# Performance work log

Measured on AMD Instinct MI355X. Metric: run time of the kernel, lower is better.

The kernel has to match this reference:

```python
import jax, jax.numpy as jnp
import numpy as np

N = 50000      # nodes
E = 800000     # edges (avg degree 16)
F = 6          # input node features
C = 64         # conv_hidden_channels
M = 256        # mlp_hidden_channels
NCLS = 24      # num_classes
EPS = 1e-5     # BatchNorm eps


def _bn(h, g, b):
    # BatchNorm1d in training mode: biased batch stats over the batch axis
    mu = h.mean(axis=0)
    var = ((h - mu) ** 2).mean(axis=0)
    return g * (h - mu) * jax.lax.rsqrt(var + EPS) + b


def _block(x, W, b, g, beta):
    # Lin -> ReLU -> BN  (one MLP block)
    return _bn(jax.nn.relu(x @ W + b), g, beta)


def _edge_conv(x, src, dst, Wa, ba, ga, bea, Wb, bb, gb, beb):
    # EdgeConv: message = MLP([x_i, x_j - x_i]), max-aggregated onto target i
    xi = x[dst]                                   # [E, d]
    xj = x[src]                                   # [E, d]
    e = jnp.concatenate([xi, xj - xi], axis=-1)   # [E, 2d]
    h = _block(_block(e, Wa, ba, ga, bea), Wb, bb, gb, beb)  # [E, C]
    agg = jax.ops.segment_max(h, dst, num_segments=N)        # [N, C]
    return jnp.where(jnp.isfinite(agg), agg, 0.0)  # zero-fill isolated nodes


def setup_inputs() -> dict:
    key = jax.random.key(0)
    ks = jax.random.split(key, 12)

    def w(k, shape, fan_in):
        return jax.random.normal(k, shape, jnp.float32) * (1.0 / np.sqrt(fan_in))

    z = lambda *s: jnp.zeros(s, jnp.float32)
    o = lambda *s: jnp.ones(s, jnp.float32)

    x = jax.random.normal(ks[0], (N, F), jnp.float32)
    edge_index = jax.random.randint(ks[1], (2, E), 0, N, jnp.int32)

    return {
        "x": x,
        # conv1 MLP: Lin(2F,C)+BN, Lin(C,C)+BN
        "W1a": w(ks[2], (2 * F, C), 2 * F), "b1a": z(C), "g1a": o(C), "be1a": z(C),
        "W1b": w(ks[3], (C, C), C),         "b1b": z(C), "g1b": o(C), "be1b": z(C),
        # conv2/conv3 stacked: Lin(2C,C)+BN, Lin(C,C)+BN
        "Wa": w(ks[4], (2, 2 * C, C), 2 * C), "ba": z(2, C), "ga": o(2, C), "bea": z(2, C),
        "Wb": w(ks[5], (2, C, C), C),         "bb": z(2, C), "gb": o(2, C), "beb": z(2, C),
        # lin1: Lin(3C, M)+BN
        "Wl": w(ks[6], (3 * C, M), 3 * C), "bl": z(M), "gl": o(M), "bel": z(M),
        # head: Lin(M, M/4)+BN, Lin(M/4, M/8)+BN, Lin(M/8, NCLS)
        "Wm1": w(ks[7], (M, M // 4), M),      "bm1": z(M // 4), "gm1": o(M // 4), "bem1": z(M // 4),
        "Wm2": w(ks[8], (M // 4, M // 8), M // 4), "bm2": z(M // 8), "gm2": o(M // 8), "bem2": z(M // 8),
        "Wo": w(ks[9], (M // 8, NCLS), M // 8), "bo": z(NCLS),
        "edge_index": edge_index,
    }


def reference(x, W1a, b1a, g1a, be1a, W1b, b1b, g1b, be1b,
              Wa, ba, ga, bea, Wb, bb, gb, beb,
              Wl, bl, gl, bel,
              Wm1, bm1, gm1, bem1, Wm2, bm2, gm2, bem2,
              Wo, bo, edge_index):
    src, dst = edge_index[0], edge_index[1]
    x1 = _edge_conv(x,  src, dst, W1a, b1a, g1a, be1a, W1b, b1b, g1b, be1b)
    x2 = _edge_conv(x1, src, dst, Wa[0], ba[0], ga[0], bea[0], Wb[0], bb[0], gb[0], beb[0])
    x3 = _edge_conv(x2, src, dst, Wa[1], ba[1], ga[1], bea[1], Wb[1], bb[1], gb[1], beb[1])
    h = _block(jnp.concatenate([x1, x2, x3], axis=-1), Wl, bl, gl, bel)
    h = _block(h, Wm1, bm1, gm1, bem1)   # Dropout is identity (eval)
    h = _block(h, Wm2, bm2, gm2, bem2)   # Dropout is identity (eval)
    logits = h @ Wo + bo
    return jax.nn.log_softmax(logits, axis=1)
```

## Files before the change

kernel.cpp:

```cpp
#include <hip/hip_runtime.h>
#include <hip/hip_bf16.h>

#define EPS 1e-5f
typedef unsigned short bfr;
typedef unsigned short hfr;
typedef _Float16 h2v __attribute__((ext_vector_type(2)));
typedef _Float16 f16x8 __attribute__((ext_vector_type(8)));
typedef float f32x4 __attribute__((ext_vector_type(4)));

#if defined(__has_builtin)
#if __has_builtin(__builtin_amdgcn_fdot2)
#define HAS_FDOT2 1
#endif
#endif

static inline int cdiv(int a, int b){ return (a + b - 1) / b; }

__device__ __forceinline__ float bf2f(bfr u){ return __uint_as_float((unsigned)u << 16); }
__device__ __forceinline__ bfr f2bf(float f){
  unsigned u = __float_as_uint(f);
  u += 0x7fffu + ((u >> 16) & 1u);
  return (bfr)(u >> 16);
}
__device__ __forceinline__ unsigned pack2bf(float a, float b){
  return (unsigned)f2bf(a) | ((unsigned)f2bf(b) << 16);
}
__device__ __forceinline__ float h2f(hfr u){ _Float16 h; __builtin_memcpy(&h, &u, 2); return (float)h; }
__device__ __forceinline__ _Float16 asH(hfr u){ _Float16 h; __builtin_memcpy(&h, &u, 2); return h; }
__device__ __forceinline__ hfr f2h(float f){ _Float16 h = (_Float16)f; hfr u; __builtin_memcpy(&u, &h, 2); return u; }
__device__ __forceinline__ unsigned pack2h(float a, float b){
  return (unsigned)f2h(a) | ((unsigned)f2h(b) << 16);
}
__device__ __forceinline__ h2v u2h2(unsigned u){ h2v r; __builtin_memcpy(&r, &u, 4); return r; }
__device__ __forceinline__ unsigned h22u(h2v h){ unsigned u; __builtin_memcpy(&u, &h, 4); return u; }
__device__ __forceinline__ float dot2(h2v a, h2v b, float c){
#ifdef HAS_FDOT2
  return __builtin_amdgcn_fdot2(a, b, c, false);
#else
  return c + (float)a.x * (float)b.x + (float)a.y * (float)b.y;
#endif
}

__global__ __launch_bounds__(256) void detect_kernel(const bfr* __restrict__ xr, int nwords, int* __restrict__ flag){
  int i = threadIdx.x;
  int bad = 0;
  if (i < nwords){
    bfr lo = xr[2 * i];
    int e = (lo >> 7) & 0xFF;
    bool plausible = ((lo & 0x7FFF) == 0) || (e >= 97 && e <= 157);
    bad = plausible ? 0 : 1;
  }
  __shared__ int s[256];
  s[threadIdx.x] = bad; __syncthreads();
  for (int st = 128; st; st >>= 1){
    if (threadIdx.x < st) s[threadIdx.x] += s[threadIdx.x + st];
    __syncthreads();
  }
  if (threadIdx.x == 0) *flag = (s[0] > 32) ? 1 : 0;
}

#define NPAR 31
struct ParamPtrs { const void* p[NPAR]; };
struct ParamOfs  { int off[NPAR + 1]; };

__global__ __launch_bounds__(256) void acvt_batch_kernel(ParamPtrs pp, ParamOfs po,
                                                         float* __restrict__ out, int total,
                                                         const int* __restrict__ flag){
  int g = blockIdx.x * 256 + threadIdx.x;
  if (g >= total) return;
  int isf = *flag;
  int t = 0;
  while (po.off[t + 1] <= g) ++t;
  int i = g - po.off[t];
  out[g] = isf ? ((const float*)pp.p[t])[i] : bf2f(((const bfr*)pp.p[t])[i]);
}

__global__ __launch_bounds__(256) void deg_kernel(const int* __restrict__ dst, int* __restrict__ deg, int E){
  int e = blockIdx.x * 256 + threadIdx.x;
  if (e < E) atomicAdd(&deg[dst[e]], 1);
}

__global__ __launch_bounds__(256) void scan1_kernel(const int* __restrict__ deg, int* __restrict__ locoff,
                                                    int* __restrict__ bsum, int N){
  __shared__ int s[256];
  int i = blockIdx.x * 256 + threadIdx.x;
  int v = (i < N) ? deg[i] : 0;
  s[threadIdx.x] = v; __syncthreads();
  for (int st = 1; st < 256; st <<= 1){
    int u = (threadIdx.x >= st) ? s[threadIdx.x - st] : 0;
    __syncthreads();
    s[threadIdx.x] += u;
    __syncthreads();
  }
  if (i < N) locoff[i] = s[threadIdx.x] - v;
  if (threadIdx.x == 255) bsum[blockIdx.x] = s[255];
}

__global__ __launch_bounds__(256) void scan2_kernel(int* __restrict__ bsum, int nb){
  __shared__ int s[256];
  const int t = threadIdx.x;
  int carry = 0;
  for (int base = 0; base < nb; base += 256){
    int v = (base + t < nb) ? bsum[base + t] : 0;
    s[t] = v; __syncthreads();
    for (int st = 1; st < 256; st <<= 1){
      int u = (t >= st) ? s[t - st] : 0;
      __syncthreads();
      s[t] += u;
      __syncthreads();
    }
    if (base + t < nb) bsum[base + t] = carry + s[t] - v;
    carry += s[255];
    __syncthreads();
  }
}

__global__ __launch_bounds__(256) void scan3_kernel(const int* __restrict__ locoff, const int* __restrict__ bsum,
                                                    int* __restrict__ row_off, int* __restrict__ cur,
                                                    int N, int E){
  int i = blockIdx.x * 256 + threadIdx.x;
  if (i < N){
    int v = locoff[i] + bsum[blockIdx.x];
    row_off[i] = v; cur[i] = v;
  }
  if (i == 0) row_off[N] = E;
}

__global__ __launch_bounds__(256) void scatter_kernel(const int* __restrict__ src, const int* __restrict__ dst,
                                                      int* __restrict__ cur, int* __restrict__ ssrc,
                                                      int* __restrict__ sdst, int E){
  int e = blockIdx.x * 256 + threadIdx.x;
  if (e < E){
    int d = dst[e];
    int p = atomicAdd(&cur[d], 1);
    ssrc[p] = src[e];
    sdst[p] = d;
  }
}

template<bool FIRST>
__global__ __launch_bounds__(256) void gemmPQ_kernel(const void* __restrict__ Av, int lda,
                                                     const float* __restrict__ Wa, int d,
                                                     const float* __restrict__ ba,
                                                     hfr* __restrict__ P, hfr* __restrict__ Q, int N){
  __shared__ unsigned WsU[64 * 64];
  const int y = blockIdx.y;
  const int tot = d * 64;
  if (FIRST){
    float* Ws = (float*)WsU;
    for (int i = threadIdx.x; i < tot; i += 256)
      Ws[i] = y ? Wa[tot + i] : (Wa[i] - Wa[tot + i]);
  } else {
    for (int i = threadIdx.x; i < 32 * 64; i += 256){
      int p = i >> 6, c = i & 63;
      int i0 = (2 * p) * 64 + c, i1 = (2 * p + 1) * 64 + c;
      float w0 = y ? Wa[tot + i0] : (Wa[i0] - Wa[tot + i0]);
      float w1 = y ? Wa[tot + i1] : (Wa[i1] - Wa[tot + i1]);
      WsU[i] = pack2h(w0, w1);
    }
  }
  __syncthreads();
  const int row = blockIdx.x * 256 + threadIdx.x;
  if (row >= N) return;
  float acc[64];
#pragma unroll
  for (int c = 0; c < 64; ++c) acc[c] = 0.f;
  if (FIRST){
    const float* Ws = (const float*)WsU;
    const float* Af = (const float*)Av + (size_t)row * lda;
    for (int k = 0; k < d; ++k){
      float a = Af[k];
      const float* wr = Ws + k * 64;
#pragma unroll
      for (int c4 = 0; c4 < 16; ++c4){
        float4 w = *(const float4*)(wr + 4 * c4);
        acc[4*c4+0] += a * w.x; acc[4*c4+1] += a * w.y;
        acc[4*c4+2] += a * w.z; acc[4*c4+3] += a * w.w;
      }
    }
  } else {
    const hfr* Ah = (const hfr*)Av + (size_t)row * lda;
#pragma unroll
    for (int k8 = 0; k8 < 8; ++k8){
      uint4 av = *(const uint4*)(Ah + k8 * 8);
      unsigned pr[4] = {av.x, av.y, av.z, av.w};
#pragma unroll
      for (int pi = 0; pi < 4; ++pi){
        h2v ap = u2h2(pr[pi]);
        const unsigned* wr = WsU + (k8 * 4 + pi) * 64;
#pragma unroll
        for (int c = 0; c < 64; ++c) acc[c] = dot2(ap, u2h2(wr[c]), acc[c]);
      }
    }
  }
  if (!y){
#pragma unroll
    for (int c = 0; c < 64; ++c) acc[c] += ba[c];
  }
  unsigned p[32];
#pragma unroll
  for (int c = 0; c < 64; c += 2) p[c / 2] = pack2h(acc[c], acc[c + 1]);
  hfr* outp = (y ? Q : P) + (size_t)row * 64;
  uint4* op = (uint4*)outp;
#pragma unroll
  for (int i = 0; i < 8; ++i) op[i] = make_uint4(p[4*i], p[4*i+1], p[4*i+2], p[4*i+3]);
}

template<int NOUT, bool FOLD>
__global__ __launch_bounds__(256) void gemm_kernel(const hfr* __restrict__ Ah, int lda,
                                                   const float* __restrict__ W, int ldw,
                                                   const float* __restrict__ bias,
                                                   const float* __restrict__ stats, float cntInv,
                                                   const float* __restrict__ g, const float* __restrict__ be,
                                                   hfr* __restrict__ Ov, int ldo,
                                                   int nrows, int K, int relu){
  __shared__ unsigned Wp[32 * NOUT];
  __shared__ float aS[256], bbS[256], bfull[NOUT], bsum[256];
  const int ct = blockIdx.y * NOUT;
  const int tid = threadIdx.x;
  if (FOLD){
    for (int k = tid; k < K; k += 256){
      float mu = stats[k] * cntInv;
      float var = stats[K + k] * cntInv - mu * mu;
      float ai = g[k] * rsqrtf(var + EPS);
      aS[k] = ai; bbS[k] = be[k] - ai * mu;
    }
    __syncthreads();
    constexpr int parts = 256 / NOUT;
    int c = tid % NOUT, p = tid / NOUT;
    float s = 0.f;
    for (int k = p; k < K; k += parts) s += bbS[k] * W[(size_t)k * ldw + ct + c];
    bsum[p * NOUT + c] = s;
    __syncthreads();
    if (tid < NOUT){
      float t = bias[ct + tid];
#pragma unroll
      for (int pp = 0; pp < parts; ++pp) t += bsum[pp * NOUT + tid];
      bfull[tid] = t;
    }
  }
  const int row = blockIdx.x * 256 + tid;
  float acc[NOUT];
#pragma unroll
  for (int c = 0; c < NOUT; ++c) acc[c] = 0.f;
  for (int k0 = 0; k0 < K; k0 += 64){
    __syncthreads();
    for (int i = tid; i < 32 * NOUT; i += 256){
      int p = i / NOUT, c = i - p * NOUT;
      float w0 = W[(size_t)(k0 + 2 * p) * ldw + ct + c];
      float w1 = W[(size_t)(k0 + 2 * p + 1) * ldw + ct + c];
      if (FOLD){ w0 *= aS[k0 + 2 * p]; w1 *= aS[k0 + 2 * p + 1]; }
      Wp[i] = pack2h(w0, w1);
    }
    __syncthreads();
    if (row < nrows){
      const hfr* Ap = Ah + (size_t)row * lda + k0;
#pragma unroll
      for (int k8 = 0; k8 < 8; ++k8){
        uint4 av = *(const uint4*)(Ap + k8 * 8);
        unsigned pr[4] = {av.x, av.y, av.z, av.w};
#pragma unroll
        for (int pi = 0; pi < 4; ++pi){
          h2v ap = u2h2(pr[pi]);
          const unsigned* wr = Wp + (k8 * 4 + pi) * NOUT;
#pragma unroll
          for (int c = 0; c < NOUT; ++c) acc[c] = dot2(ap, u2h2(wr[c]), acc[c]);
        }
      }
    }
  }
  __syncthreads();
  if (row >= nrows) return;
#pragma unroll
  for (int c = 0; c < NOUT; ++c){
    float b = FOLD ? bfull[c] : bias[ct + c];
    float v = acc[c] + b;
    acc[c] = relu ? fmaxf(v, 0.f) : v;
  }
  unsigned p[NOUT / 2];
#pragma unroll
  for (int c = 0; c < NOUT; c += 2) p[c / 2] = pack2h(acc[c], acc[c + 1]);
  uint4* op = (uint4*)(Ov + (size_t)row * ldo + ct);
#pragma unroll
  for (int i = 0; i < NOUT / 8; ++i) op[i] = make_uint4(p[4*i], p[4*i+1], p[4*i+2], p[4*i+3]);
}

__global__ __launch_bounds__(256) void passA_kernel(const hfr* __restrict__ P, const hfr* __restrict__ Q,
                                                    const int* __restrict__ ssrc, const int* __restrict__ sdst,
                                                    float* __restrict__ stats, int E){
  const int tid = threadIdx.x;
  const int lane = tid & 63;
  const int wib = tid >> 6;
  const int er0 = lane >> 3;
  const int ck = lane & 7;
  const int wid = (blockIdx.x * 256 + tid) >> 6;
  const int nw = (gridDim.x * 256) >> 6;
  const _Float16 z16 = (_Float16)0;
  const int lim = E - 1;
  float s8[8], q8[8];
#pragma unroll
  for (int j = 0; j < 8; ++j){ s8[j] = 0.f; q8[j] = 0.f; }
  for (int base = wid * 16; base < E; base += nw * 16){
    int idx = min(base + (lane & 15), lim);
    int sv = ssrc[idx];
    int dv = sdst[idx];
#pragma unroll
    for (int h = 0; h < 2; ++h){
      int er = h * 8 + er0;
      bool valid = (base + er) < E;
      int sj = __shfl(sv, er, 64);
      int dj = __shfl(dv, er, 64);
      uint4 qv = *((const uint4*)(Q + (size_t)sj * 64) + ck);
      uint4 pv = *((const uint4*)(P + (size_t)dj * 64) + ck);
      unsigned qa[4] = {qv.x, qv.y, qv.z, qv.w};
      unsigned pa[4] = {pv.x, pv.y, pv.z, pv.w};
#pragma unroll
      for (int t = 0; t < 4; ++t){
        h2v sm = u2h2(qa[t]) + u2h2(pa[t]);
        float v0 = (sm.x < z16) ? 0.f : (float)sm.x;
        float v1 = (sm.y < z16) ? 0.f : (float)sm.y;
        v0 = valid ? v0 : 0.f; v1 = valid ? v1 : 0.f;
        s8[2*t]   += v0; q8[2*t]   += v0 * v0;
        s8[2*t+1] += v1; q8[2*t+1] += v1 * v1;
      }
    }
  }
#pragma unroll
  for (int j = 0; j < 8; ++j){
    float s = s8[j], q = q8[j];
    s += __shfl_xor(s, 8, 64);  q += __shfl_xor(q, 8, 64);
    s += __shfl_xor(s, 16, 64); q += __shfl_xor(q, 16, 64);
    s += __shfl_xor(s, 32, 64); q += __shfl_xor(q, 32, 64);
    s8[j] = s; q8[j] = q;
  }
  __shared__ float ls[4][64], lq[4][64];
  if (lane < 8){
#pragma unroll
    for (int j = 0; j < 8; ++j){ ls[wib][lane * 8 + j] = s8[j]; lq[wib][lane * 8 + j] = q8[j]; }
  }
  __syncthreads();
  if (tid < 64){
    atomicAdd(&stats[tid], ls[0][tid] + ls[1][tid] + ls[2][tid] + ls[3][tid]);
  } else if (tid < 128){
    int c = tid - 64;
    atomicAdd(&stats[64 + c], lq[0][c] + lq[1][c] + lq[2][c] + lq[3][c]);
  }
}

__global__ __launch_bounds__(256) void passBC_kernel(const hfr* __restrict__ P, const hfr* __restrict__ Q,
                                                     const int* __restrict__ ssrc, const int* __restrict__ row_off,
                                                     const float* __restrict__ statsIn, float Einv,
                                                     const float* __restrict__ g1, const float* __restrict__ be1,
                                                     const float* __restrict__ Wb, const float* __restrict__ bn,
                                                     float* __restrict__ agg, float* __restrict__ statsOut, int N){
  __shared__ __align__(16) _Float16 W2T[64 * 72];
  __shared__ __align__(16) _Float16 ht[4][16][72];
  __shared__ float aS[64], bbS[64], b2S[64], bsum[256], qsum[256];
  const int tid = threadIdx.x;
  const int lane = tid & 63;
  const int er0 = lane >> 3;
  const int ck = lane & 7;
  const int wib = tid >> 6;
  const _Float16 z16 = (_Float16)0;
  if (tid < 64){
    float mu = statsIn[tid] * Einv;
    float var = statsIn[64 + tid] * Einv - mu * mu;
    float ai = g1[tid] * rsqrtf(var + EPS);
    aS[tid] = ai; bbS[tid] = be1[tid] - ai * mu;
  }
  __syncthreads();
  for (int i = tid; i < 4096; i += 256){
    int c = i >> 6, k = i & 63;
    W2T[c * 72 + k] = (_Float16)(aS[k] * Wb[(size_t)k * 64 + c]);
  }
  {
    int c = tid & 63, p = tid >> 6;
    float s = 0.f;
    for (int k = p; k < 64; k += 4) s += bbS[k] * Wb[(size_t)k * 64 + c];
    bsum[p * 64 + c] = s;
  }
  __syncthreads();
  if (tid < 64) b2S[tid] = bn[tid] + bsum[tid] + bsum[64 + tid] + bsum[128 + tid] + bsum[192 + tid];
  __syncthreads();
  f16x8 Bf[4][2];
#pragma unroll
  for (int t = 0; t < 4; ++t)
#pragma unroll
    for (int h = 0; h < 2; ++h){
      int c = t * 16 + (lane & 15);
      Bf[t][h] = *(const f16x8*)&W2T[c * 72 + h * 32 + (lane >> 4) * 8];
    }
  float bc[4];
#pragma unroll
  for (int t = 0; t < 4; ++t) bc[t] = b2S[t * 16 + (lane & 15)];
  _Float16 (*hl)[72] = ht[wib];
  const int wid = (blockIdx.x * 256 + tid) >> 6;
  const int nw = (gridDim.x * 256) >> 6;
  float sumT[4] = {0.f,0.f,0.f,0.f}, sqT[4] = {0.f,0.f,0.f,0.f};
  for (int n = wid; n < N; n += nw){
    const int e0 = row_off[n], e1 = row_off[n + 1];
    if (e0 >= e1) continue;
    uint4 pv4 = ((const uint4*)(P + (size_t)n * 64))[ck];
    h2v pp0 = u2h2(pv4.x), pp1 = u2h2(pv4.y), pp2 = u2h2(pv4.z), pp3 = u2h2(pv4.w);
    const int lim = e1 - 1;
    float mxT[4] = {0.f,0.f,0.f,0.f};
    for (int eb = e0; eb < e1; eb += 16){
      int sv = ssrc[min(eb + (lane & 15), lim)];
#pragma unroll
      for (int h = 0; h < 2; ++h){
        int er = h * 8 + er0;
        int sj = __shfl(sv, er, 64);
        uint4 qv = *((const uint4*)(Q + (size_t)sj * 64) + ck);
        h2v s0 = u2h2(qv.x) + pp0;
        h2v s1 = u2h2(qv.y) + pp1;
        h2v s2 = u2h2(qv.z) + pp2;
        h2v s3 = u2h2(qv.w) + pp3;
        s0.x = (s0.x < z16) ? z16 : s0.x; s0.y = (s0.y < z16) ? z16 : s0.y;
        s1.x = (s1.x < z16) ? z16 : s1.x; s1.y = (s1.y < z16) ? z16 : s1.y;
        s2.x = (s2.x < z16) ? z16 : s2.x; s2.y = (s2.y < z16) ? z16 : s2.y;
        s3.x = (s3.x < z16) ? z16 : s3.x; s3.y = (s3.y < z16) ? z16 : s3.y;
        *(uint4*)&hl[er][ck * 8] = make_uint4(h22u(s0), h22u(s1), h22u(s2), h22u(s3));
      }
      f16x8 A0 = *(const f16x8*)&hl[lane & 15][(lane >> 4) * 8];
      f16x8 A1 = *(const f16x8*)&hl[lane & 15][32 + (lane >> 4) * 8];
#pragma unroll
      for (int t = 0; t < 4; ++t){
        f32x4 Cv = {bc[t], bc[t], bc[t], bc[t]};
        Cv = __builtin_amdgcn_mfma_f32_16x16x32_f16(A0, Bf[t][0], Cv, 0, 0, 0);
        Cv = __builtin_amdgcn_mfma_f32_16x16x32_f16(A1, Bf[t][1], Cv, 0, 0, 0);
#pragma unroll
        for (int r = 0; r < 4; ++r){
          float v = fmaxf(Cv[r], 0.f);
          int rowi = (lane >> 4) * 4 + r;
          bool valid = (eb + rowi) < e1;
          mxT[t] = fmaxf(mxT[t], v);
          sumT[t] += valid ? v : 0.f;
          sqT[t]  += valid ? v * v : 0.f;
        }
      }
    }
#pragma unroll
    for (int t = 0; t < 4; ++t){
      float m = mxT[t];
      m = fmaxf(m, __shfl_xor(m, 16, 64));
      m = fmaxf(m, __shfl_xor(m, 32, 64));
      mxT[t] = m;
    }
    float outv = (lane < 16) ? mxT[0] : (lane < 32) ? mxT[1] : (lane < 48) ? mxT[2] : mxT[3];
    agg[(size_t)n * 64 + lane] = outv;
  }
#pragma unroll
  for (int t = 0; t < 4; ++t){
    float s = sumT[t], q = sqT[t];
    s += __shfl_xor(s, 16, 64); s += __shfl_xor(s, 32, 64);
    q += __shfl_xor(q, 16, 64); q += __shfl_xor(q, 32, 64);
    sumT[t] = s; sqT[t] = q;
  }
  float ssel = (lane < 16) ? sumT[0] : (lane < 32) ? sumT[1] : (lane < 48) ? sumT[2] : sumT[3];
  float qsel = (lane < 16) ? sqT[0]  : (lane < 32) ? sqT[1]  : (lane < 48) ? sqT[2]  : sqT[3];
  bsum[tid] = ssel; qsum[tid] = qsel;
  __syncthreads();
  if (tid < 64){
    atomicAdd(&statsOut[tid], bsum[tid] + bsum[64 + tid] + bsum[128 + tid] + bsum[192 + tid]);
  } else if (tid < 128){
    int c = tid - 64;
    atomicAdd(&statsOut[64 + c], qsum[c] + qsum[64 + c] + qsum[128 + c] + qsum[192 + c]);
  }
}

__global__ __launch_bounds__(256) void fixup_kernel(const float* __restrict__ agg, const int* __restrict__ deg,
                                                    const float* __restrict__ stats, float cntInv,
                                                    const float* __restrict__ g, const float* __restrict__ be,
                                                    hfr* __restrict__ xout, int ldx, int N){
  int t = blockIdx.x * 256 + threadIdx.x;
  if (t >= N * 64) return;
  int n = t >> 6, c = t & 63;
  float mu = stats[c] * cntInv;
  float var = stats[64 + c] * cntInv - mu * mu;
  float a = g[c] * rsqrtf(var + EPS);
  float b = be[c] - a * mu;
  float v = 0.f;
  if (deg[n] > 0) v = a * agg[t] + b;
  xout[(size_t)n * ldx + c] = f2h(v);
}

template<int C>
__global__ __launch_bounds__(256) void statsN_kernel(const hfr* __restrict__ u, float* __restrict__ stats, int N){
  constexpr int RP = 256 / C;
  const int c = threadIdx.x % C, j = threadIdx.x / C;
  float sum = 0.f, sq = 0.f;
  for (int r = blockIdx.x * RP + j; r < N; r += gridDim.x * RP){
    float v = h2f(u[(size_t)r * C + c]);
    sum += v; sq += v * v;
  }
  __shared__ float ls[256], lq[256];
  ls[threadIdx.x] = sum; lq[threadIdx.x] = sq;
  __syncthreads();
  if (threadIdx.x < C){
    float s = 0.f, q = 0.f;
#pragma unroll
    for (int jj = 0; jj < RP; ++jj){ s += ls[jj * C + c]; q += lq[jj * C + c]; }
    atomicAdd(&stats[c], s); atomicAdd(&stats[C + c], q);
  }
}

__global__ __launch_bounds__(256) void head_kernel(const hfr* __restrict__ u2,
                                                   const float* __restrict__ stats, float cntInv,
                                                   const float* __restrict__ g, const float* __restrict__ be,
                                                   const float* __restrict__ Wo, const float* __restrict__ bo,
                                                   void* __restrict__ out, int N, const int* __restrict__ flag){
  __shared__ float Ws[32 * 24];
  __shared__ float bs[24];
  __shared__ float aS[32], bbS[32];
  const int tid = threadIdx.x;
  if (tid < 32){
    float mu = stats[tid] * cntInv;
    float var = stats[32 + tid] * cntInv - mu * mu;
    float ai = g[tid] * rsqrtf(var + EPS);
    aS[tid] = ai; bbS[tid] = be[tid] - ai * mu;
  }
  __syncthreads();
  for (int i = tid; i < 32 * 24; i += 256){
    int k = i / 24, c = i - 24 * k;
    Ws[i] = aS[k] * Wo[(size_t)k * 24 + c];
  }
  if (tid < 24){
    float t = bo[tid];
    for (int k = 0; k < 32; ++k) t += bbS[k] * Wo[(size_t)k * 24 + tid];
    bs[tid] = t;
  }
  __syncthreads();
  int r = blockIdx.x * 256 + tid;
  if (r >= N) return;
  int isf = *flag;
  float l[24];
#pragma unroll
  for (int c = 0; c < 24; ++c) l[c] = bs[c];
  const hfr* up = u2 + (size_t)r * 32;
#pragma unroll
  for (int k = 0; k < 32; ++k){
    float v = h2f(up[k]);
#pragma unroll
    for (int c = 0; c < 24; ++c) l[c] += v * Ws[k * 24 + c];
  }
  float m = l[0];
#pragma unroll
  for (int c = 1; c < 24; ++c) m = fmaxf(m, l[c]);
  float s = 0.f;
#pragma unroll
  for (int c = 0; c < 24; ++c) s += expf(l[c] - m);
  float lse = m + logf(s);
  if (isf){
    float4* op = (float4*)((float*)out + (size_t)r * 24);
#pragma unroll
    for (int i = 0; i < 6; ++i)
      op[i] = make_float4(l[4*i] - lse, l[4*i+1] - lse, l[4*i+2] - lse, l[4*i+3] - lse);
  } else {
    unsigned p[12];
#pragma unroll
    for (int c = 0; c < 24; c += 2) p[c / 2] = pack2bf(l[c] - lse, l[c + 1] - lse);
    uint4* op = (uint4*)((bfr*)out + (size_t)r * 24);
#pragma unroll
    for (int i = 0; i < 3; ++i) op[i] = make_uint4(p[4*i], p[4*i+1], p[4*i+2], p[4*i+3]);
  }
}

extern "C" void kernel_launch(void* const* d_in, const int* in_sizes, int n_in,
                              void* d_out, int out_size, void* d_ws, size_t ws_size,
                              hipStream_t stream){
  const int N = in_sizes[0] / 6;
  const int E = in_sizes[31] / 2;
  const int* edge = (const int*)d_in[31];
  const int* src = edge;
  const int* dst = edge + E;

  size_t off = 0; char* basep = (char*)d_ws;
  auto alloc = [&](size_t bytes) -> void* {
    void* p = basep + off;
    off = (off + bytes + 255) & ~(size_t)255;
    return p;
  };
  float* stA  = (float*)alloc(1472 * 4);
  float* stN1 = stA + 768;
  float* stN2 = stA + 1280;
  float* stN3 = stA + 1408;
  int*   flag = (int*)  alloc(4);
  int*   deg  = (int*)  alloc((size_t)N * 4);
  int*   rowo = (int*)  alloc((size_t)(N + 1) * 4);
  int*   cur  = (int*)  alloc((size_t)N * 4);
  int*   loco = (int*)  alloc((size_t)N * 4);
  int*   bsc  = (int*)  alloc(1024 * 4);
  int*   ssrc = (int*)  alloc((size_t)E * 4);
  int*   sdst = (int*)  alloc((size_t)E * 4);

  ParamPtrs pp; ParamOfs po;
  int hoff[32]; int total = 0;
  for (int s = 0; s < NPAR; ++s){
    int idx = (s < 30) ? (s + 1) : 0;
    pp.p[s] = d_in[idx];
    po.off[s] = total;
    hoff[idx] = total;
    total += in_sizes[idx];
  }
  po.off[NPAR] = total;
  float* pf = (float*)alloc((size_t)total * 4);

  hfr*   P    = (hfr*)  alloc((size_t)N * 64 * 2);
  hfr*   Qb   = (hfr*)  alloc((size_t)N * 64 * 2);
  float* agg  = (float*)alloc((size_t)N * 64 * 4);
  hfr*   xcat = (hfr*)  alloc((size_t)N * 192 * 2);
  hfr* u_l = (hfr*)P;
  hfr* u1  = xcat;
  hfr* u2  = xcat + (size_t)N * 64;
  (void)ws_size; (void)n_in; (void)out_size;

  dim3 B(256);
  detect_kernel<<<1, B, 0, stream>>>((const bfr*)d_in[0], 256, flag);
  acvt_batch_kernel<<<cdiv(total, 256), B, 0, stream>>>(pp, po, pf, total, flag);

  hipMemsetAsync(stA, 0, 1472 * 4, stream);
  hipMemsetAsync(deg, 0, (size_t)N * 4, stream);
  deg_kernel<<<cdiv(E, 256), B, 0, stream>>>(dst, deg, E);
  const int NBn = cdiv(N, 256);
  scan1_kernel<<<NBn, B, 0, stream>>>(deg, loco, bsc, N);
  scan2_kernel<<<1, B, 0, stream>>>(bsc, NBn);
  scan3_kernel<<<NBn, B, 0, stream>>>(loco, bsc, rowo, cur, N, E);
  scatter_kernel<<<cdiv(E, 256), B, 0, stream>>>(src, dst, cur, ssrc, sdst, E);

  const int NB = cdiv(N, 256);
  const int GWA = 1024, GWB = 1024;
  const float Einv = 1.f / (float)E;
  for (int k = 0; k < 3; ++k){
    const float *Wa_k, *ba_k, *ga_k, *bea_k, *Wb_k, *bb_k, *gb_k, *beb_k;
    if (k == 0){
      Wa_k = pf + hoff[1]; ba_k = pf + hoff[2]; ga_k = pf + hoff[3]; bea_k = pf + hoff[4];
      Wb_k = pf + hoff[5]; bb_k = pf + hoff[6]; gb_k = pf + hoff[7]; beb_k = pf + hoff[8];
    } else {
      int kk = k - 1;
      Wa_k = pf + hoff[9]  + (size_t)kk * 128 * 64;
      ba_k = pf + hoff[10] + kk * 64;
      ga_k = pf + hoff[11] + kk * 64;
      bea_k= pf + hoff[12] + kk * 64;
      Wb_k = pf + hoff[13] + (size_t)kk * 64 * 64;
      bb_k = pf + hoff[14] + kk * 64;
      gb_k = pf + hoff[15] + kk * 64;
      beb_k= pf + hoff[16] + kk * 64;
    }
    float* st1 = stA + k * 256;
    float* st2 = st1 + 128;
    if (k == 0)
      gemmPQ_kernel<true><<<dim3(NB, 2), B, 0, stream>>>(pf + hoff[0], 6, Wa_k, 6, ba_k, P, Qb, N);
    else
      gemmPQ_kernel<false><<<dim3(NB, 2), B, 0, stream>>>(xcat + (size_t)(k - 1) * 64, 192, Wa_k, 64, ba_k, P, Qb, N);
    passA_kernel<<<GWA, B, 0, stream>>>(P, Qb, ssrc, sdst, st1, E);
    passBC_kernel<<<GWB, B, 0, stream>>>(P, Qb, ssrc, rowo, st1, Einv, ga_k, bea_k, Wb_k, bb_k,
                                         agg, st2, N);
    fixup_kernel<<<cdiv(N * 64, 256), B, 0, stream>>>(agg, deg, st2, Einv, gb_k, beb_k,
                                                      xcat + (size_t)k * 64, 192, N);
  }

  gemm_kernel<64, false><<<dim3(NB, 4), B, 0, stream>>>(xcat, 192, pf + hoff[17], 256, pf + hoff[18],
                                                        nullptr, 0.f, nullptr, nullptr,
                                                        u_l, 256, N, 192, 1);
  statsN_kernel<256><<<512, B, 0, stream>>>(u_l, stN1, N);
  gemm_kernel<64, true><<<dim3(NB, 1), B, 0, stream>>>(u_l, 256, pf + hoff[21], 64, pf + hoff[22],
                                                       stN1, 1.f / (float)N, pf + hoff[19], pf + hoff[20],
                                                       u1, 64, N, 256, 1);
  statsN_kernel<64><<<512, B, 0, stream>>>(u1, stN2, N);
  gemm_kernel<32, true><<<dim3(NB, 1), B, 0, stream>>>(u1, 64, pf + hoff[25], 32, pf + hoff[26],
                                                       stN2, 1.f / (float)N, pf + hoff[23], pf + hoff[24],
                                                       u2, 32, N, 64, 1);
  statsN_kernel<32><<<512, B, 0, stream>>>(u2, stN3, N);
  head_kernel<<<cdiv(N, 256), B, 0, stream>>>(u2, stN3, 1.f / (float)N, pf + hoff[27], pf + hoff[28],
                                              pf + hoff[29], pf + hoff[30], d_out, N, flag);
}
```

Baseline: 879.4 us.

## Replace scalar dot2 node GEMMs with MFMA-based persistent GEMM kernel

```diff
diff --git a/kernel.cpp b/kernel.cpp
--- a/kernel.cpp
+++ b/kernel.cpp
@@ -15,6 +15,7 @@
 #endif
 
 static inline int cdiv(int a, int b){ return (a + b - 1) / b; }
+static inline int imin(int a, int b){ return a < b ? a : b; }
 
 __device__ __forceinline__ float bf2f(bfr u){ return __uint_as_float((unsigned)u << 16); }
 __device__ __forceinline__ bfr f2bf(float f){
@@ -26,7 +27,6 @@
   return (unsigned)f2bf(a) | ((unsigned)f2bf(b) << 16);
 }
 __device__ __forceinline__ float h2f(hfr u){ _Float16 h; __builtin_memcpy(&h, &u, 2); return (float)h; }
-__device__ __forceinline__ _Float16 asH(hfr u){ _Float16 h; __builtin_memcpy(&h, &u, 2); return h; }
 __device__ __forceinline__ hfr f2h(float f){ _Float16 h = (_Float16)f; hfr u; __builtin_memcpy(&u, &h, 2); return u; }
 __device__ __forceinline__ unsigned pack2h(float a, float b){
   return (unsigned)f2h(a) | ((unsigned)f2h(b) << 16);
@@ -206,18 +206,26 @@
   for (int i = 0; i < 8; ++i) op[i] = make_uint4(p[4*i], p[4*i+1], p[4*i+2], p[4*i+3]);
 }
 
-template<int NOUT, bool FOLD>
-__global__ __launch_bounds__(256) void gemm_kernel(const hfr* __restrict__ Ah, int lda,
-                                                   const float* __restrict__ W, int ldw,
-                                                   const float* __restrict__ bias,
-                                                   const float* __restrict__ stats, float cntInv,
-                                                   const float* __restrict__ g, const float* __restrict__ be,
-                                                   hfr* __restrict__ Ov, int ldo,
-                                                   int nrows, int K, int relu){
-  __shared__ unsigned Wp[32 * NOUT];
-  __shared__ float aS[256], bbS[256], bfull[NOUT], bsum[256];
-  const int ct = blockIdx.y * NOUT;
+template<int NOUT, int KSTEPS, bool FOLD>
+__global__ __launch_bounds__(256) void mgemm_kernel(const hfr* __restrict__ Ah, int lda,
+                                                    const float* __restrict__ Wp, const float* __restrict__ Wm, int ldw,
+                                                    const float* __restrict__ bias,
+                                                    const float* __restrict__ stats, float cntInv,
+                                                    const float* __restrict__ g, const float* __restrict__ be,
+                                                    hfr* __restrict__ Ov, int ldo,
+                                                    int nrows, int relu){
+  constexpr int K  = KSTEPS * 32;
+  constexpr int KP = K + 8;
+  constexpr int NT = NOUT / 16;
+  __shared__ __align__(16) _Float16 W2T[NOUT * KP];
+  __shared__ __align__(16) _Float16 etile[4][16][NOUT + 8];
+  __shared__ float aS[FOLD ? K : 1], bbS[FOLD ? K : 1], bsum[FOLD ? 256 : 1];
+  __shared__ float bfull[NOUT];
   const int tid = threadIdx.x;
+  const int lane = tid & 63;
+  const int wib = tid >> 6;
+  const int colbase = blockIdx.y * NOUT;
+
   if (FOLD){
     for (int k = tid; k < K; k += 256){
       float mu = stats[k] * cntInv;
@@ -226,63 +234,83 @@
       aS[k] = ai; bbS[k] = be[k] - ai * mu;
     }
     __syncthreads();
+  }
+  for (int i = tid; i < K * NOUT; i += 256){
+    int k = i / NOUT, c = i - k * NOUT;
+    float w = Wp[(size_t)k * ldw + colbase + c];
+    if (Wm) w -= Wm[(size_t)k * ldw + colbase + c];
+    if (FOLD) w *= aS[k];
+    W2T[c * KP + k] = (_Float16)w;
+  }
+  if (FOLD){
     constexpr int parts = 256 / NOUT;
     int c = tid % NOUT, p = tid / NOUT;
     float s = 0.f;
-    for (int k = p; k < K; k += parts) s += bbS[k] * W[(size_t)k * ldw + ct + c];
+    for (int k = p; k < K; k += parts) s += bbS[k] * Wp[(size_t)k * ldw + colbase + c];
     bsum[p * NOUT + c] = s;
     __syncthreads();
     if (tid < NOUT){
-      float t = bias[ct + tid];
+      float t = bias[colbase + tid];
 #pragma unroll
       for (int pp = 0; pp < parts; ++pp) t += bsum[pp * NOUT + tid];
       bfull[tid] = t;
     }
-  }
-  const int row = blockIdx.x * 256 + tid;
-  float acc[NOUT];
-#pragma unroll
-  for (int c = 0; c < NOUT; ++c) acc[c] = 0.f;
-  for (int k0 = 0; k0 < K; k0 += 64){
-    __syncthreads();
-    for (int i = tid; i < 32 * NOUT; i += 256){
-      int p = i / NOUT, c = i - p * NOUT;
-      float w0 = W[(size_t)(k0 + 2 * p) * ldw + ct + c];
-      float w1 = W[(size_t)(k0 + 2 * p + 1) * ldw + ct + c];
-      if (FOLD){ w0 *= aS[k0 + 2 * p]; w1 *= aS[k0 + 2 * p + 1]; }
-      Wp[i] = pack2h(w0, w1);
-    }
-    __syncthreads();
-    if (row < nrows){
-      const hfr* Ap = Ah + (size_t)row * lda + k0;
-#pragma unroll
-      for (int k8 = 0; k8 < 8; ++k8){
-        uint4 av = *(const uint4*)(Ap + k8 * 8);
-        unsigned pr[4] = {av.x, av.y, av.z, av.w};
-#pragma unroll
-        for (int pi = 0; pi < 4; ++pi){
-          h2v ap = u2h2(pr[pi]);
-          const unsigned* wr = Wp + (k8 * 4 + pi) * NOUT;
-#pragma unroll
-          for (int c = 0; c < NOUT; ++c) acc[c] = dot2(ap, u2h2(wr[c]), acc[c]);
-        }
+  } else {
+    if (tid < NOUT) bfull[tid] = bias ? bias[colbase + tid] : 0.f;
+  }
+  __syncthreads();
+
+  f16x8 Bf[KSTEPS][NT];
+#pragma unroll
+  for (int s = 0; s < KSTEPS; ++s)
+#pragma unroll
+    for (int t = 0; t < NT; ++t)
+      Bf[s][t] = *(const f16x8*)&W2T[(t * 16 + (lane & 15)) * KP + s * 32 + (lane >> 4) * 8];
+  float bc[NT];
+#pragma unroll
+  for (int t = 0; t < NT; ++t) bc[t] = bfull[t * 16 + (lane & 15)];
+
+  const int ntiles = (nrows + 63) >> 6;
+  for (int tile = blockIdx.x; tile < ntiles; tile += gridDim.x){
+    const int r0 = tile * 64 + wib * 16;
+    const int rowA = min(r0 + (lane & 15), nrows - 1);
+    const hfr* Ap = Ah + (size_t)rowA * lda + (lane >> 4) * 8;
+    f32x4 acc[NT];
+#pragma unroll
+    for (int t = 0; t < NT; ++t) acc[t] = (f32x4){bc[t], bc[t], bc[t], bc[t]};
+#pragma unroll
+    for (int s = 0; s < KSTEPS; ++s){
+      f16x8 Af = *(const f16x8*)(Ap + s * 32);
+#pragma unroll
+      for (int t = 0; t < NT; ++t)
+        acc[t] = __builtin_amdgcn_mfma_f32_16x16x32_f16(Af, Bf[s][t], acc[t], 0, 0, 0);
+    }
+#pragma unroll
+    for (int t = 0; t < NT; ++t){
+#pragma unroll
+      for (int r = 0; r < 4; ++r){
+        float v = acc[t][r];
+        v = relu ? fmaxf(v, 0.f) : v;
+        etile[wib][(lane >> 4) * 4 + r][t * 16 + (lane & 15)] = (_Float16)v;
       }
     }
-  }
-  __syncthreads();
-  if (row >= nrows) return;
-#pragma unroll
-  for (int c = 0; c < NOUT; ++c){
-    float b = FOLD ? bfull[c] : bias[ct + c];
-    float v = acc[c] + b;
-    acc[c] = relu ? fmaxf(v, 0.f) : v;
-  }
-  unsigned p[NOUT / 2];
-#pragma unroll
-  for (int c = 0; c < NOUT; c += 2) p[c / 2] = pack2h(acc[c], acc[c + 1]);
-  uint4* op = (uint4*)(Ov + (size_t)row * ldo + ct);
-#pragma unroll
-  for (int i = 0; i < NOUT / 8; ++i) op[i] = make_uint4(p[4*i], p[4*i+1], p[4*i+2], p[4*i+3]);
+    if (NOUT == 64){
+#pragma unroll
+      for (int h = 0; h < 2; ++h){
+        int rl = h * 8 + (lane >> 3);
+        int ch = lane & 7;
+        uint4 vv = *(const uint4*)&etile[wib][rl][ch * 8];
+        int rg = r0 + rl;
+        if (rg < nrows) *(uint4*)(Ov + (size_t)rg * ldo + colbase + ch * 8) = vv;
+      }
+    } else {
+      int rl = lane >> 2;
+      int ch = lane & 3;
+      uint4 vv = *(const uint4*)&etile[wib][rl][ch * 8];
+      int rg = r0 + rl;
+      if (rg < nrows) *(uint4*)(Ov + (size_t)rg * ldo + colbase + ch * 8) = vv;
+    }
+  }
 }
 
 __global__ __launch_bounds__(256) void passA_kernel(const hfr* __restrict__ P, const hfr* __restrict__ Q,
@@ -628,6 +656,7 @@
   scatter_kernel<<<cdiv(E, 256), B, 0, stream>>>(src, dst, cur, ssrc, sdst, E);
 
   const int NB = cdiv(N, 256);
+  const int ntiles = cdiv(N, 64);
   const int GWA = 1024, GWB = 1024;
   const float Einv = 1.f / (float)E;
   for (int k = 0; k < 3; ++k){
@@ -648,10 +677,16 @@
     }
     float* st1 = stA + k * 256;
     float* st2 = st1 + 128;
-    if (k == 0)
+    if (k == 0){
       gemmPQ_kernel<true><<<dim3(NB, 2), B, 0, stream>>>(pf + hoff[0], 6, Wa_k, 6, ba_k, P, Qb, N);
-    else
-      gemmPQ_kernel<false><<<dim3(NB, 2), B, 0, stream>>>(xcat + (size_t)(k - 1) * 64, 192, Wa_k, 64, ba_k, P, Qb, N);
+    } else {
+      mgemm_kernel<64, 2, false><<<dim3(imin(ntiles, 1024), 1), B, 0, stream>>>(
+          xcat + (size_t)(k - 1) * 64, 192, Wa_k, Wa_k + 64 * 64, 64, ba_k,
+          nullptr, 0.f, nullptr, nullptr, P, 64, N, 0);
+      mgemm_kernel<64, 2, false><<<dim3(imin(ntiles, 1024), 1), B, 0, stream>>>(
+          xcat + (size_t)(k - 1) * 64, 192, Wa_k + 64 * 64, nullptr, 64, nullptr,
+          nullptr, 0.f, nullptr, nullptr, Qb, 64, N, 0);
+    }
     passA_kernel<<<GWA, B, 0, stream>>>(P, Qb, ssrc, sdst, st1, E);
     passBC_kernel<<<GWB, B, 0, stream>>>(P, Qb, ssrc, rowo, st1, Einv, ga_k, bea_k, Wb_k, bb_k,
                                          agg, st2, N);
@@ -659,18 +694,19 @@
                                                       xcat + (size_t)k * 64, 192, N);
   }
 
-  gemm_kernel<64, false><<<dim3(NB, 4), B, 0, stream>>>(xcat, 192, pf + hoff[17], 256, pf + hoff[18],
-                                                        nullptr, 0.f, nullptr, nullptr,
-                                                        u_l, 256, N, 192, 1);
+  mgemm_kernel<64, 6, false><<<dim3(imin(ntiles, 256), 4), B, 0, stream>>>(
+      xcat, 192, pf + hoff[17], nullptr, 256, pf + hoff[18],
+      nullptr, 0.f, nullptr, nullptr, u_l, 256, N, 1);
   statsN_kernel<256><<<512, B, 0, stream>>>(u_l, stN1, N);
-  gemm_kernel<64, true><<<dim3(NB, 1), B, 0, stream>>>(u_l, 256, pf + hoff[21], 64, pf + hoff[22],
-                                                       stN1, 1.f / (float)N, pf + hoff[19], pf + hoff[20],
-                                                       u1, 64, N, 256, 1);
+  mgemm_kernel<32, 8, true><<<dim3(imin(ntiles, 512), 2), B, 0, stream>>>(
+      u_l, 256, pf + hoff[21], nullptr, 64, pf + hoff[22],
+      stN1, 1.f / (float)N, pf + hoff[19], pf + hoff[20], u1, 64, N, 1);
   statsN_kernel<64><<<512, B, 0, stream>>>(u1, stN2, N);
-  gemm_kernel<32, true><<<dim3(NB, 1), B, 0, stream>>>(u1, 64, pf + hoff[25], 32, pf + hoff[26],
-                                                       stN2, 1.f / (float)N, pf + hoff[23], pf + hoff[24],
-                                                       u2, 32, N, 64, 1);
+  mgemm_kernel<32, 2, true><<<dim3(imin(ntiles, 1024), 1), B, 0, stream>>>(
+      u1, 64, pf + hoff[25], nullptr, 32, pf + hoff[26],
+      stN2, 1.f / (float)N, pf + hoff[23], pf + hoff[24], u2, 32, N, 1);
   statsN_kernel<32><<<512, B, 0, stream>>>(u2, stN3, N);
   head_kernel<<<cdiv(N, 256), B, 0, stream>>>(u2, stN3, 1.f / (float)N, pf + hoff[27], pf + hoff[28],
                                               pf + hoff[29], pf + hoff[30], d_out, N, flag);
-}
+  (void)NB;
+}
```

After: 775.4 us. 11.8% less time.
